# Kernel tuning notes

Measured on AMD Instinct MI355X. Metric: run time of the kernel, lower is better.

## Reference

```python
import jax, jax.numpy as jnp
from jax import lax
import numpy as np

MAXDISP = 48
KSIZE = 5
DILATION = 2


def _im2col(z, k, dil):
    # z: [N,1,H,W] -> patches [N, k*k, H, W], same H,W via symmetric padding
    pad = dil * (k - 1) // 2
    return lax.conv_general_dilated_patches(
        z,
        filter_shape=(k, k),
        window_strides=(1, 1),
        padding=[(pad, pad), (pad, pad)],
        rhs_dilation=(dil, dil),
    )


def setup_inputs() -> dict:
    key = jax.random.key(0)
    k1, k2, k3, k4 = jax.random.split(key, 4)
    N, C, H, W = 2, 32, 128, 256
    x = jax.random.normal(k1, (N, C, H, W), dtype=jnp.float32)
    y = jax.random.normal(k2, (N, C, H, W), dtype=jnp.float32)
    filters = jax.random.normal(k3, (N, KSIZE * KSIZE, H, W), dtype=jnp.float32)
    filters_biases = jax.random.normal(k4, (N, 1, H, W), dtype=jnp.float32)
    return {"x": x, "y": y, "filters": filters, "filters_biases": filters_biases}


def reference(x, y, filters, filters_biases):
    N, C, H, W = x.shape
    D = MAXDISP
    # left-pad right feature with D-1 zeros along width
    y_pad = jnp.pad(y, ((0, 0), (0, 0), (0, 0), (D - 1, 0)))
    bias = filters_biases[:, 0]  # [N,H,W]

    def step(carry, start):
        y_sl = lax.dynamic_slice_in_dim(y_pad, start, W, axis=3)  # [N,C,H,W]
        z = jnp.sum(x * y_sl, axis=1, keepdims=True)              # [N,1,H,W]
        p = _im2col(z, KSIZE, DILATION)                            # [N,k*k,H,W]
        out = jnp.sum(p * filters, axis=1) + bias                  # [N,H,W]
        return carry, out

    # disparity i uses slice start D-1-i (torch loop runs d = D-1 .. 0)
    starts = (D - 1) - jnp.arange(D)
    _, corr = lax.scan(step, None, starts)   # [D,N,H,W]
    return jnp.transpose(corr, (1, 0, 2, 3))  # [N,D,H,W]
```

## Files before the change

### kernel.cpp

```cpp
#include <hip/hip_runtime.h>

#define NB 2
#define C 32
#define H 128
#define W 256
#define D 48
#define HW (H * W)

__global__ __launch_bounds__(192) void zkern(const float* __restrict__ x,
                                             const float* __restrict__ y,
                                             float* __restrict__ z) {
    const int b    = blockIdx.x;
    const int half = b & 1;
    const int nh   = b >> 1;
    const int n    = nh / H;
    const int h    = nh % H;
    const int tid  = threadIdx.x;
    const int q    = tid & 31;
    const int dg   = tid >> 5;
    const int d0   = dg * 8;

    __shared__ __align__(16) float ys[C][184];

    const float* xrow = x + ((size_t)(n * C) * H + h) * (size_t)W;
    const float* yrow = y + ((size_t)(n * C) * H + h) * (size_t)W;
    const int ybase = 128 * half - 48;

#pragma unroll
    for (int it = 0; it < 8; ++it) {
        const int idx = it * 192 + tid;
        if (idx < 32 * 46) {
            const int r    = idx / 46;
            const int c4   = idx % 46;
            const int yidx = ybase + 4 * c4;
            float4 v = {0.f, 0.f, 0.f, 0.f};
            if (yidx >= 0 && yidx <= W - 4)
                v = *(const float4*)(yrow + (size_t)r * HW + yidx);
            *(float4*)&ys[r][4 * c4] = v;
        }
    }
    __syncthreads();

    float acc[8][4] = {};
    const int S0 = 4 * q + 40 - d0;

#pragma unroll
    for (int c = 0; c < C; ++c) {
        const float4 xv = *(const float4*)(xrow + (size_t)c * HW + 128 * half + 4 * q);
        const float4 w0 = *(const float4*)&ys[c][S0];
        const float4 w1 = *(const float4*)&ys[c][S0 + 4];
        const float4 w2 = *(const float4*)&ys[c][S0 + 8];
        const float win[12] = {w0.x, w0.y, w0.z, w0.w,
                               w1.x, w1.y, w1.z, w1.w,
                               w2.x, w2.y, w2.z, w2.w};
        const float xs[4] = {xv.x, xv.y, xv.z, xv.w};
#pragma unroll
        for (int k = 0; k < 8; ++k)
#pragma unroll
            for (int o = 0; o < 4; ++o)
                acc[k][o] += xs[o] * win[8 + o - k];
    }

    float* zp = z + (((size_t)n * D + d0) * H + h) * (size_t)W + 128 * half + 4 * q;
#pragma unroll
    for (int k = 0; k < 8; ++k) {
        float4 v;
        v.x = acc[k][0]; v.y = acc[k][1]; v.z = acc[k][2]; v.w = acc[k][3];
        *(float4*)(zp + (size_t)k * HW) = v;
    }
}

#define DCH 8
#define NCH (D / DCH)

__global__ __launch_bounds__(256) void fkern(const float* __restrict__ z,
                                             const float* __restrict__ Ff,
                                             const float* __restrict__ B,
                                             float* __restrict__ out) {
    __shared__ __align__(16) float zs[DCH][5][264];

    const int b  = blockIdx.x;
    const int ch = b % NCH;
    const int nh = b / NCH;
    const int n  = nh / H;
    const int h  = nh % H;
    const int tid = threadIdx.x;
    const int q  = tid & 63;
    const int g  = tid >> 6;
    const int d0 = ch * DCH;

#pragma unroll
    for (int it = 0; it < 11; ++it) {
        const int idx = it * 256 + tid;
        if (idx < 40 * 66) {
            const int r  = idx / 66;
            const int c4 = idx % 66;
            const int dd = r / 5;
            const int i  = r % 5;
            const int hh = h + 2 * i - 4;
            float4 v = {0.f, 0.f, 0.f, 0.f};
            if (c4 >= 1 && c4 <= 64 && hh >= 0 && hh < H)
                v = *(const float4*)(z + (((size_t)n * D + d0 + dd) * H + hh) * (size_t)W
                                       + 4 * c4 - 4);
            *(float4*)&zs[dd][i][4 * c4] = v;
        }
    }

    const float4 bias = *(const float4*)(B + ((size_t)n * H + h) * (size_t)W + 4 * q);
    float acc[2][4];
#pragma unroll
    for (int kd = 0; kd < 2; ++kd) {
        acc[kd][0] = bias.x; acc[kd][1] = bias.y;
        acc[kd][2] = bias.z; acc[kd][3] = bias.w;
    }

    __syncthreads();

#pragma unroll
    for (int i = 0; i < 5; ++i) {
        float4 f[5];
#pragma unroll
        for (int jj = 0; jj < 5; ++jj)
            f[jj] = *(const float4*)(Ff + (((size_t)n * 25 + i * 5 + jj) * H + h) * (size_t)W
                                        + 4 * q);
        const float fs[5][4] = {
            {f[0].x, f[0].y, f[0].z, f[0].w},
            {f[1].x, f[1].y, f[1].z, f[1].w},
            {f[2].x, f[2].y, f[2].z, f[2].w},
            {f[3].x, f[3].y, f[3].z, f[3].w},
            {f[4].x, f[4].y, f[4].z, f[4].w}};

#pragma unroll
        for (int kd = 0; kd < 2; ++kd) {
            const int dd = g + 4 * kd;
            const float4 w0 = *(const float4*)&zs[dd][i][4 * q];
            const float4 w1 = *(const float4*)&zs[dd][i][4 * q + 4];
            const float4 w2 = *(const float4*)&zs[dd][i][4 * q + 8];
            const float win[12] = {w0.x, w0.y, w0.z, w0.w,
                                   w1.x, w1.y, w1.z, w1.w,
                                   w2.x, w2.y, w2.z, w2.w};
#pragma unroll
            for (int jj = 0; jj < 5; ++jj)
#pragma unroll
                for (int o = 0; o < 4; ++o)
                    acc[kd][o] += fs[jj][o] * win[o + 2 * jj];
        }
    }

#pragma unroll
    for (int kd = 0; kd < 2; ++kd) {
        float* op = out + (((size_t)n * D + d0 + g + 4 * kd) * H + h) * (size_t)W + 4 * q;
        float4 v;
        v.x = acc[kd][0]; v.y = acc[kd][1]; v.z = acc[kd][2]; v.w = acc[kd][3];
        *(float4*)op = v;
    }
}

__global__ __launch_bounds__(256) void fused_naive(const float* __restrict__ x,
                                                   const float* __restrict__ y,
                                                   const float* __restrict__ Ff,
                                                   const float* __restrict__ B,
                                                   float* __restrict__ out) {
    const size_t idx = (size_t)blockIdx.x * 256 + threadIdx.x;
    if (idx >= (size_t)NB * D * H * W) return;
    const int w = (int)(idx % W);
    const int h = (int)((idx / W) % H);
    const int d = (int)((idx / ((size_t)W * H)) % D);
    const int n = (int)(idx / ((size_t)W * H * D));

    float acc = B[((size_t)n * H + h) * W + w];
#pragma unroll
    for (int i = 0; i < 5; ++i) {
        const int hh = h + 2 * i - 4;
        if (hh < 0 || hh >= H) continue;
#pragma unroll
        for (int j = 0; j < 5; ++j) {
            const int ww = w + 2 * j - 4;
            if (ww < 0 || ww >= W) continue;
            const int ws_ = ww - d;
            float zv = 0.f;
            if (ws_ >= 0) {
                const float* xp = x + (((size_t)n * C) * H + hh) * (size_t)W + ww;
                const float* yp = y + (((size_t)n * C) * H + hh) * (size_t)W + ws_;
                for (int c = 0; c < C; ++c)
                    zv += xp[(size_t)c * HW] * yp[(size_t)c * HW];
            }
            acc += Ff[(((size_t)n * 25 + i * 5 + j) * H + h) * (size_t)W + w] * zv;
        }
    }
    out[idx] = acc;
}

extern "C" void kernel_launch(void* const* d_in, const int* in_sizes, int n_in,
                              void* d_out, int out_size, void* d_ws, size_t ws_size,
                              hipStream_t stream) {
    const float* x = (const float*)d_in[0];
    const float* y = (const float*)d_in[1];
    const float* F = (const float*)d_in[2];
    const float* B = (const float*)d_in[3];
    float* out = (float*)d_out;

    const size_t zbytes = (size_t)NB * D * H * W * sizeof(float);

    if (ws_size >= zbytes) {
        float* z = (float*)d_ws;
        zkern<<<NB * H * 2, 192, 0, stream>>>(x, y, z);
        fkern<<<NB * H * NCH, 256, 0, stream>>>(z, F, B, out);
    } else {
        const size_t total = (size_t)NB * D * H * W;
        fused_naive<<<(int)((total + 255) / 256), 256, 0, stream>>>(x, y, F, B, out);
    }
}
```

Baseline: 32.71 us.

## Share z halo rows across two output rows in filter kernel, prefetch x

```diff
diff --git a/kernel.cpp b/kernel.cpp
--- a/kernel.cpp
+++ b/kernel.cpp
@@ -7,9 +7,9 @@
 #define D 48
 #define HW (H * W)
 
-__global__ __launch_bounds__(192) void zkern(const float* __restrict__ x,
-                                             const float* __restrict__ y,
-                                             float* __restrict__ z) {
+__global__ __launch_bounds__(192, 2) void zkern(const float* __restrict__ x,
+                                                const float* __restrict__ y,
+                                                float* __restrict__ z) {
     const int b    = blockIdx.x;
     const int half = b & 1;
     const int nh   = b >> 1;
@@ -44,9 +44,13 @@
     float acc[8][4] = {};
     const int S0 = 4 * q + 40 - d0;
 
+    const float* xcol = xrow + 128 * half + 4 * q;
+    float4 xv = *(const float4*)xcol;
+
 #pragma unroll
     for (int c = 0; c < C; ++c) {
-        const float4 xv = *(const float4*)(xrow + (size_t)c * HW + 128 * half + 4 * q);
+        float4 xn = xv;
+        if (c < C - 1) xn = *(const float4*)(xcol + (size_t)(c + 1) * HW);
         const float4 w0 = *(const float4*)&ys[c][S0];
         const float4 w1 = *(const float4*)&ys[c][S0 + 4];
         const float4 w2 = *(const float4*)&ys[c][S0 + 8];
@@ -59,6 +63,7 @@
 #pragma unroll
             for (int o = 0; o < 4; ++o)
                 acc[k][o] += xs[o] * win[8 + o - k];
+        xv = xn;
     }
 
     float* zp = z + (((size_t)n * D + d0) * H + h) * (size_t)W + 128 * half + 4 * q;
@@ -73,87 +78,93 @@
 #define DCH 8
 #define NCH (D / DCH)
 
-__global__ __launch_bounds__(256) void fkern(const float* __restrict__ z,
-                                             const float* __restrict__ Ff,
-                                             const float* __restrict__ B,
-                                             float* __restrict__ out) {
-    __shared__ __align__(16) float zs[DCH][5][264];
-
-    const int b  = blockIdx.x;
-    const int ch = b % NCH;
-    const int nh = b / NCH;
-    const int n  = nh / H;
-    const int h  = nh % H;
+__global__ __launch_bounds__(256, 3) void fkern(const float* __restrict__ z,
+                                                const float* __restrict__ Ff,
+                                                const float* __restrict__ B,
+                                                float* __restrict__ out) {
+    __shared__ __align__(16) float zs[DCH][6][264];
+
+    int b = blockIdx.x;
+    const int ch = b % NCH;  b /= NCH;
+    const int pi = b % 32;   b /= 32;
+    const int p  = b % 2;    b /= 2;
+    const int n  = b;
+    const int h0 = 4 * pi + p;
+    const int d0 = ch * DCH;
+
     const int tid = threadIdx.x;
-    const int q  = tid & 63;
-    const int g  = tid >> 6;
-    const int d0 = ch * DCH;
-
-#pragma unroll
-    for (int it = 0; it < 11; ++it) {
+    const int q   = tid & 63;
+    const int g   = tid >> 6;
+
+#pragma unroll
+    for (int it = 0; it < 13; ++it) {
         const int idx = it * 256 + tid;
-        if (idx < 40 * 66) {
-            const int r  = idx / 66;
+        if (idx < 48 * 66) {
             const int c4 = idx % 66;
-            const int dd = r / 5;
-            const int i  = r % 5;
-            const int hh = h + 2 * i - 4;
+            const int t2 = idx / 66;
+            const int l  = t2 % 6;
+            const int dd = t2 / 6;
+            const int hh = h0 - 4 + 2 * l;
             float4 v = {0.f, 0.f, 0.f, 0.f};
             if (c4 >= 1 && c4 <= 64 && hh >= 0 && hh < H)
                 v = *(const float4*)(z + (((size_t)n * D + d0 + dd) * H + hh) * (size_t)W
                                        + 4 * c4 - 4);
-            *(float4*)&zs[dd][i][4 * c4] = v;
-        }
-    }
-
-    const float4 bias = *(const float4*)(B + ((size_t)n * H + h) * (size_t)W + 4 * q);
-    float acc[2][4];
-#pragma unroll
-    for (int kd = 0; kd < 2; ++kd) {
-        acc[kd][0] = bias.x; acc[kd][1] = bias.y;
-        acc[kd][2] = bias.z; acc[kd][3] = bias.w;
+            *(float4*)&zs[dd][l][4 * c4] = v;
+        }
+    }
+
+    float acc[2][2][4];
+#pragma unroll
+    for (int r = 0; r < 2; ++r) {
+        const float4 bv = *(const float4*)(B + ((size_t)n * H + h0 + 2 * r) * (size_t)W + 4 * q);
+        acc[r][0][0] = bv.x; acc[r][0][1] = bv.y; acc[r][0][2] = bv.z; acc[r][0][3] = bv.w;
+        acc[r][1][0] = bv.x; acc[r][1][1] = bv.y; acc[r][1][2] = bv.z; acc[r][1][3] = bv.w;
     }
 
     __syncthreads();
 
 #pragma unroll
-    for (int i = 0; i < 5; ++i) {
-        float4 f[5];
-#pragma unroll
-        for (int jj = 0; jj < 5; ++jj)
-            f[jj] = *(const float4*)(Ff + (((size_t)n * 25 + i * 5 + jj) * H + h) * (size_t)W
-                                        + 4 * q);
-        const float fs[5][4] = {
-            {f[0].x, f[0].y, f[0].z, f[0].w},
-            {f[1].x, f[1].y, f[1].z, f[1].w},
-            {f[2].x, f[2].y, f[2].z, f[2].w},
-            {f[3].x, f[3].y, f[3].z, f[3].w},
-            {f[4].x, f[4].y, f[4].z, f[4].w}};
-
+    for (int l = 0; l < 6; ++l) {
+        const float4 a0 = *(const float4*)&zs[g][l][4 * q];
+        const float4 a1 = *(const float4*)&zs[g][l][4 * q + 4];
+        const float4 a2 = *(const float4*)&zs[g][l][4 * q + 8];
+        const float4 b0 = *(const float4*)&zs[g + 4][l][4 * q];
+        const float4 b1 = *(const float4*)&zs[g + 4][l][4 * q + 4];
+        const float4 b2 = *(const float4*)&zs[g + 4][l][4 * q + 8];
+        const float win0[12] = {a0.x, a0.y, a0.z, a0.w, a1.x, a1.y, a1.z, a1.w,
+                                a2.x, a2.y, a2.z, a2.w};
+        const float win1[12] = {b0.x, b0.y, b0.z, b0.w, b1.x, b1.y, b1.z, b1.w,
+                                b2.x, b2.y, b2.z, b2.w};
+
+#pragma unroll
+        for (int r = 0; r < 2; ++r) {
+            const int i = l - r;
+            if (i < 0 || i > 4) continue;
+#pragma unroll
+            for (int jj = 0; jj < 5; ++jj) {
+                const float4 tp = *(const float4*)(Ff + (((size_t)n * 25 + i * 5 + jj) * H
+                                                         + h0 + 2 * r) * (size_t)W + 4 * q);
+                const float ts[4] = {tp.x, tp.y, tp.z, tp.w};
+#pragma unroll
+                for (int o = 0; o < 4; ++o) {
+                    acc[r][0][o] += ts[o] * win0[o + 2 * jj];
+                    acc[r][1][o] += ts[o] * win1[o + 2 * jj];
+                }
+            }
+        }
+    }
+
+#pragma unroll
+    for (int r = 0; r < 2; ++r)
 #pragma unroll
         for (int kd = 0; kd < 2; ++kd) {
-            const int dd = g + 4 * kd;
-            const float4 w0 = *(const float4*)&zs[dd][i][4 * q];
-            const float4 w1 = *(const float4*)&zs[dd][i][4 * q + 4];
-            const float4 w2 = *(const float4*)&zs[dd][i][4 * q + 8];
-            const float win[12] = {w0.x, w0.y, w0.z, w0.w,
-                                   w1.x, w1.y, w1.z, w1.w,
-                                   w2.x, w2.y, w2.z, w2.w};
-#pragma unroll
-            for (int jj = 0; jj < 5; ++jj)
-#pragma unroll
-                for (int o = 0; o < 4; ++o)
-                    acc[kd][o] += fs[jj][o] * win[o + 2 * jj];
-        }
-    }
-
-#pragma unroll
-    for (int kd = 0; kd < 2; ++kd) {
-        float* op = out + (((size_t)n * D + d0 + g + 4 * kd) * H + h) * (size_t)W + 4 * q;
-        float4 v;
-        v.x = acc[kd][0]; v.y = acc[kd][1]; v.z = acc[kd][2]; v.w = acc[kd][3];
-        *(float4*)op = v;
-    }
+            float* op = out + (((size_t)n * D + d0 + g + 4 * kd) * H + h0 + 2 * r) * (size_t)W
+                            + 4 * q;
+            float4 v;
+            v.x = acc[r][kd][0]; v.y = acc[r][kd][1];
+            v.z = acc[r][kd][2]; v.w = acc[r][kd][3];
+            *(float4*)op = v;
+        }
 }
 
 __global__ __launch_bounds__(256) void fused_naive(const float* __restrict__ x,
@@ -205,7 +216,7 @@
     if (ws_size >= zbytes) {
         float* z = (float*)d_ws;
         zkern<<<NB * H * 2, 192, 0, stream>>>(x, y, z);
-        fkern<<<NB * H * NCH, 256, 0, stream>>>(z, F, B, out);
+        fkern<<<NB * 2 * 32 * NCH, 256, 0, stream>>>(z, F, B, out);
     } else {
         const size_t total = (size_t)NB * D * H * W;
         fused_naive<<<(int)((total + 255) / 256), 256, 0, stream>>>(x, y, F, B, out);
```

New measurement: 35.57 us. 8.7% more time.
